# Optimization experiments

Measured on AMD Instinct MI355X. Metric: run time of the kernel, lower is better.

Reference implementation:

```python
import jax, jax.numpy as jnp
import numpy as np

T, B, I, H = 4096, 32, 128, 128


def setup_inputs() -> dict:
    key = jax.random.key(0)
    ks = jax.random.split(key, 8)
    return {
        "input": jax.random.normal(ks[0], (T, B, I), dtype=jnp.float32),
        "h0": jax.random.normal(ks[1], (B, H), dtype=jnp.float32),
        "c0": jax.random.normal(ks[2], (B, H), dtype=jnp.float32),
        "noise": jax.random.normal(ks[3], (B, H), dtype=jnp.float32),
        "W_ih": jax.random.normal(ks[4], (4 * H, I), dtype=jnp.float32) * 0.05,
        "W_hh": jax.random.normal(ks[5], (4 * H, H), dtype=jnp.float32) * 0.05,
        "b_ih": jax.random.normal(ks[6], (4 * H,), dtype=jnp.float32) * 0.05,
        "b_hh": jax.random.normal(ks[7], (4 * H,), dtype=jnp.float32) * 0.05,
    }


def reference(input, h0, c0, noise, W_ih, W_hh, b_ih, b_hh):
    # NOTE: the source LSTMLayer never rebinds `state` inside its loop, so every
    # timestep applies the cell to the SAME initial (h0, c0). This is therefore a
    # time-batched (non-recurrent) LSTM-cell application -> fully vectorized over T.
    hsz = h0.shape[-1]
    # gates: [T, B, 4H]
    gates = (
        jnp.einsum("tbi,gi->tbg", input, W_ih)
        + jnp.einsum("bh,gh->bg", h0, W_hh)[None, :, :]
        + (b_ih + b_hh)
    )
    i_g = jax.nn.sigmoid(gates[..., 0 * hsz : 1 * hsz])
    f_g = jax.nn.sigmoid(gates[..., 1 * hsz : 2 * hsz])
    g_g = jnp.tanh(gates[..., 2 * hsz : 3 * hsz])
    o_g = jax.nn.sigmoid(gates[..., 3 * hsz : 4 * hsz])
    c = f_g * c0[None] + i_g * g_g               # [T, B, H]
    h = o_g * jnp.tanh(c) + noise[None]          # [T, B, H] (additive process noise)
    outputs = h
    # (h, c) returned by the torch loop are those of the LAST iteration
    return (outputs, (h[-1], c[-1]))
```

## Files before the change

kernel.cpp:

```cpp
#include <hip/hip_runtime.h>
#include <hip/hip_bf16.h>

#define T_DIM 4096
#define B_DIM 32
#define H_DIM 128
#define M_DIM (T_DIM * B_DIM)
#define G_DIM 512
#define TBH   ((long)M_DIM * H_DIM)

#define RPB    512
#define NCHUNK (RPB / 32)
#define LSTR   136
#define LBUF   (32 * LSTR)

typedef __attribute__((ext_vector_type(8))) short short8;
typedef __attribute__((ext_vector_type(4))) short short4v;
typedef __attribute__((ext_vector_type(4))) float floatx4;

__device__ __forceinline__ unsigned short f2bf_rne(float x) {
    union { float f; unsigned int u; } v; v.f = x;
    unsigned int r = v.u + 0x7FFFu + ((v.u >> 16) & 1u);
    return (unsigned short)(r >> 16);
}
__device__ __forceinline__ unsigned short f2bf_rh(float x) {
    union { float f; unsigned int u; } v; v.f = x;
    return (unsigned short)((v.u + 0x8000u) >> 16);
}
__device__ __forceinline__ float sigm(float x) {
    return __builtin_amdgcn_rcpf(1.0f + __expf(-x));
}
__device__ __forceinline__ float tanh_fast(float x) {
    float e = __expf(-2.0f * __builtin_fabsf(x));
    float t = (1.0f - e) * __builtin_amdgcn_rcpf(1.0f + e);
    return __builtin_copysignf(t, x);
}
__device__ __forceinline__ short8 pack8(float4 f0, float4 f1) {
    short8 s;
    s[0] = (short)f2bf_rh(f0.x); s[1] = (short)f2bf_rh(f0.y);
    s[2] = (short)f2bf_rh(f0.z); s[3] = (short)f2bf_rh(f0.w);
    s[4] = (short)f2bf_rh(f1.x); s[5] = (short)f2bf_rh(f1.y);
    s[6] = (short)f2bf_rh(f1.z); s[7] = (short)f2bf_rh(f1.w);
    return s;
}

__global__ void prep(const float* __restrict__ h0,
                     const float* __restrict__ W_hh,
                     const float* __restrict__ b_ih,
                     const float* __restrict__ b_hh,
                     const float* __restrict__ W_ih,
                     unsigned short* __restrict__ Wb,
                     float* __restrict__ hh) {
    const int tid = threadIdx.x;
    if (blockIdx.x < 32) {
        __shared__ float h0s[128];
        const int b = blockIdx.x;
        if (tid < 128) h0s[tid] = h0[b * 128 + tid];
        __syncthreads();
        for (int g = tid; g < G_DIM; g += 256) {
            float acc = b_ih[g] + b_hh[g];
            const float* wr = W_hh + g * 128;
            #pragma unroll 8
            for (int k = 0; k < 128; ++k) acc += wr[k] * h0s[k];
            hh[b * G_DIM + g] = acc;
        }
    } else {
        const int e = ((blockIdx.x - 32) * 256 + tid) * 4;
        float4 f = *(const float4*)(W_ih + e);
        short4v s;
        s[0] = (short)f2bf_rne(f.x); s[1] = (short)f2bf_rne(f.y);
        s[2] = (short)f2bf_rne(f.z); s[3] = (short)f2bf_rne(f.w);
        *(short4v*)(Wb + e) = s;
    }
}

__global__ __launch_bounds__(512, 2) void lstm_main(
    const float* __restrict__ X,
    const unsigned short* __restrict__ W,
    const float* __restrict__ hh,
    const float* __restrict__ c0,
    const float* __restrict__ noise,
    float* __restrict__ out)
{
    __shared__ unsigned short Xs[2 * LBUF];

    const int tid  = threadIdx.x;
    const int w    = tid >> 6;
    const int lane = tid & 63;
    const int q    = lane >> 4;
    const int lr   = lane & 15;
    const int hcol = (w << 4) + lr;
    const long row0 = (long)blockIdx.x * RPB;

    short8 wf[4][4];
    #pragma unroll
    for (int g = 0; g < 4; ++g)
        #pragma unroll
        for (int kt = 0; kt < 4; ++kt)
            wf[g][kt] = *(const short8*)(W + (g * 128 + hcol) * 128 + kt * 32 + q * 8);

    floatx4 hhf[2][4];
    float c0v[2][4], nzv[2][4];
    #pragma unroll
    for (int mt = 0; mt < 2; ++mt) {
        #pragma unroll
        for (int r = 0; r < 4; ++r) {
            const int b = mt * 16 + q * 4 + r;
            c0v[mt][r] = c0[b * 128 + hcol];
            nzv[mt][r] = noise[b * 128 + hcol];
        }
        #pragma unroll
        for (int g = 0; g < 4; ++g) {
            floatx4 a;
            #pragma unroll
            for (int r = 0; r < 4; ++r)
                a[r] = hh[(mt * 16 + q * 4 + r) * G_DIM + g * 128 + hcol];
            hhf[mt][g] = a;
        }
    }

    const int srow = tid >> 4;
    const int scol = (tid & 15) << 3;
    const float* xsrc = X + (row0 + srow) * 128 + scol;
    unsigned short* lws = &Xs[srow * LSTR + scol];

    {
        float4 f0 = *(const float4*)(xsrc);
        float4 f1 = *(const float4*)(xsrc + 4);
        *(short8*)lws = pack8(f0, f1);
    }
    float4 p0 = *(const float4*)(xsrc + 4096);
    float4 p1 = *(const float4*)(xsrc + 4096 + 4);
    __syncthreads();

    for (int c = 0; c < NCHUNK; ++c) {
        float4 n0 = {}, n1 = {};
        if (c + 2 < NCHUNK) {
            n0 = *(const float4*)(xsrc + (long)(c + 2) * 4096);
            n1 = *(const float4*)(xsrc + (long)(c + 2) * 4096 + 4);
        }

        const unsigned short* rb = &Xs[(c & 1) * LBUF];
        short8 af[2][4];
        #pragma unroll
        for (int mt = 0; mt < 2; ++mt)
            #pragma unroll
            for (int kt = 0; kt < 4; ++kt)
                af[mt][kt] = *(const short8*)(rb + (mt * 16 + lr) * LSTR + kt * 32 + q * 8);

        floatx4 acc[2][4];
        #pragma unroll
        for (int mt = 0; mt < 2; ++mt)
            #pragma unroll
            for (int g = 0; g < 4; ++g)
                acc[mt][g] = hhf[mt][g];

        #pragma unroll
        for (int kt = 0; kt < 4; ++kt)
            #pragma unroll
            for (int g = 0; g < 4; ++g) {
                acc[0][g] = __builtin_amdgcn_mfma_f32_16x16x32_bf16(af[0][kt], wf[g][kt], acc[0][g], 0, 0, 0);
                acc[1][g] = __builtin_amdgcn_mfma_f32_16x16x32_bf16(af[1][kt], wf[g][kt], acc[1][g], 0, 0, 0);
            }

        const long rbase = row0 + (long)c * 32;
        const bool last = (rbase == M_DIM - 32);
        #pragma unroll
        for (int mt = 0; mt < 2; ++mt)
            #pragma unroll
            for (int r = 0; r < 4; ++r) {
                const long row = rbase + mt * 16 + q * 4 + r;
                const float gi = sigm(acc[mt][0][r]);
                const float gf = sigm(acc[mt][1][r]);
                const float gg = tanh_fast(acc[mt][2][r]);
                const float go = sigm(acc[mt][3][r]);
                const float cc = gf * c0v[mt][r] + gi * gg;
                const float hv = go * tanh_fast(cc) + nzv[mt][r];
                out[row * 128 + hcol] = hv;
                if (last) {
                    const int b = mt * 16 + q * 4 + r;
                    out[TBH +        b * 128 + hcol] = hv;
                    out[TBH + 4096 + b * 128 + hcol] = cc;
                }
            }

        if (c + 1 < NCHUNK)
            *(short8*)(lws + ((c + 1) & 1) * LBUF) = pack8(p0, p1);
        __syncthreads();
        p0 = n0; p1 = n1;
    }
}

extern "C" void kernel_launch(void* const* d_in, const int* in_sizes, int n_in,
                              void* d_out, int out_size, void* d_ws, size_t ws_size,
                              hipStream_t stream) {
    const float* X     = (const float*)d_in[0];
    const float* h0    = (const float*)d_in[1];
    const float* c0    = (const float*)d_in[2];
    const float* noise = (const float*)d_in[3];
    const float* W_ih  = (const float*)d_in[4];
    const float* W_hh  = (const float*)d_in[5];
    const float* b_ih  = (const float*)d_in[6];
    const float* b_hh  = (const float*)d_in[7];

    unsigned short* Wb = (unsigned short*)d_ws;
    float* hh = (float*)((char*)d_ws + 512 * 128 * sizeof(unsigned short));
    float* out = (float*)d_out;

    prep<<<dim3(96), dim3(256), 0, stream>>>(h0, W_hh, b_ih, b_hh, W_ih, Wb, hh);
    lstm_main<<<dim3(M_DIM / RPB), dim3(512), 0, stream>>>(X, Wb, hh, c0, noise, out);
}
```

Before: 150.6 us.

## Software-pipeline MFMA of next chunk with epilogue of previous chunk

Restructures the main loop into a two-accumulator ping-pong so the MFMA for chunk c+1 is issued before the transcendental epilogue and stores of chunk c. The aim is to overlap matrix-core work with VALU activation math and global stores, which the old loop ran back-to-back. It doubles the live accumulator registers, which may raise VGPR pressure under launch_bounds(512,2) and risk spills or lower occupancy.

```diff
diff --git a/kernel.cpp b/kernel.cpp
--- a/kernel.cpp
+++ b/kernel.cpp
@@ -16,6 +16,8 @@
 typedef __attribute__((ext_vector_type(8))) short short8;
 typedef __attribute__((ext_vector_type(4))) short short4v;
 typedef __attribute__((ext_vector_type(4))) float floatx4;
+
+struct F8 { float4 a, b; };
 
 __device__ __forceinline__ unsigned short f2bf_rne(float x) {
     union { float f; unsigned int u; } v; v.f = x;
@@ -123,37 +125,28 @@
     const float* xsrc = X + (row0 + srow) * 128 + scol;
     unsigned short* lws = &Xs[srow * LSTR + scol];
 
-    {
-        float4 f0 = *(const float4*)(xsrc);
-        float4 f1 = *(const float4*)(xsrc + 4);
-        *(short8*)lws = pack8(f0, f1);
-    }
-    float4 p0 = *(const float4*)(xsrc + 4096);
-    float4 p1 = *(const float4*)(xsrc + 4096 + 4);
-    __syncthreads();
-
-    for (int c = 0; c < NCHUNK; ++c) {
-        float4 n0 = {}, n1 = {};
-        if (c + 2 < NCHUNK) {
-            n0 = *(const float4*)(xsrc + (long)(c + 2) * 4096);
-            n1 = *(const float4*)(xsrc + (long)(c + 2) * 4096 + 4);
-        }
-
-        const unsigned short* rb = &Xs[(c & 1) * LBUF];
+    auto loadX = [&](int c) -> F8 {
+        F8 v;
+        v.a = *(const float4*)(xsrc + (long)c * 4096);
+        v.b = *(const float4*)(xsrc + (long)c * 4096 + 4);
+        return v;
+    };
+    auto stage_write = [&](int par, F8 v) {
+        *(short8*)(lws + par * LBUF) = pack8(v.a, v.b);
+    };
+    auto mfma_chunk = [&](floatx4 (&acc)[2][4], int par) {
+        const unsigned short* rb = &Xs[par * LBUF];
         short8 af[2][4];
         #pragma unroll
         for (int mt = 0; mt < 2; ++mt)
             #pragma unroll
             for (int kt = 0; kt < 4; ++kt)
                 af[mt][kt] = *(const short8*)(rb + (mt * 16 + lr) * LSTR + kt * 32 + q * 8);
-
-        floatx4 acc[2][4];
         #pragma unroll
         for (int mt = 0; mt < 2; ++mt)
             #pragma unroll
             for (int g = 0; g < 4; ++g)
                 acc[mt][g] = hhf[mt][g];
-
         #pragma unroll
         for (int kt = 0; kt < 4; ++kt)
             #pragma unroll
@@ -161,8 +154,8 @@
                 acc[0][g] = __builtin_amdgcn_mfma_f32_16x16x32_bf16(af[0][kt], wf[g][kt], acc[0][g], 0, 0, 0);
                 acc[1][g] = __builtin_amdgcn_mfma_f32_16x16x32_bf16(af[1][kt], wf[g][kt], acc[1][g], 0, 0, 0);
             }
-
-        const long rbase = row0 + (long)c * 32;
+    };
+    auto epilogue = [&](const floatx4 (&acc)[2][4], long rbase) {
         const bool last = (rbase == M_DIM - 32);
         #pragma unroll
         for (int mt = 0; mt < 2; ++mt)
@@ -182,12 +175,43 @@
                     out[TBH + 4096 + b * 128 + hcol] = cc;
                 }
             }
-
-        if (c + 1 < NCHUNK)
-            *(short8*)(lws + ((c + 1) & 1) * LBUF) = pack8(p0, p1);
+    };
+
+    floatx4 accA[2][4], accB[2][4];
+
+    {
+        F8 v0;
+        v0.a = *(const float4*)(xsrc);
+        v0.b = *(const float4*)(xsrc + 4);
+        stage_write(0, v0);
+    }
+    F8 p = loadX(1);
+    __syncthreads();
+    mfma_chunk(accA, 0);
+    stage_write(1, p);
+    p = loadX(2);
+    __syncthreads();
+
+    #pragma unroll 1
+    for (int c = 1; c + 2 < NCHUNK; c += 2) {
+        F8 n = loadX(c + 2);
+        mfma_chunk(accB, 1);
+        epilogue(accA, row0 + (long)(c - 1) * 32);
+        stage_write(0, p);
         __syncthreads();
-        p0 = n0; p1 = n1;
-    }
+        p = n;
+        F8 n2 = {};
+        if (c + 3 < NCHUNK) n2 = loadX(c + 3);
+        mfma_chunk(accA, 0);
+        epilogue(accB, row0 + (long)c * 32);
+        stage_write(1, p);
+        __syncthreads();
+        p = n2;
+    }
+
+    mfma_chunk(accB, 1);
+    epilogue(accA, row0 + (long)(NCHUNK - 2) * 32);
+    epilogue(accB, row0 + (long)(NCHUNK - 1) * 32);
 }
 
 extern "C" void kernel_launch(void* const* d_in, const int* in_sizes, int n_in,
```

New measurement: 150.5 us. No clear change (-0.1%).

## Split hidden columns across two blocks with 256 threads each

Applied to the files above, without the earlier changes.

Each block now handles 64 of the 128 hidden columns using 4 waves instead of 8, and the grid doubles to cover both column halves. Each thread stages 16 input elements per chunk instead of 8. The intent is more blocks in flight for better occupancy and latency hiding. The cost is that each input row chunk is read and converted to bf16 by two blocks, doubling X traffic into the caches.

```diff
diff --git a/kernel.cpp b/kernel.cpp
--- a/kernel.cpp
+++ b/kernel.cpp
@@ -73,7 +73,7 @@
     }
 }
 
-__global__ __launch_bounds__(512, 2) void lstm_main(
+__global__ __launch_bounds__(256, 2) void lstm_main(
     const float* __restrict__ X,
     const unsigned short* __restrict__ W,
     const float* __restrict__ hh,
@@ -88,8 +88,9 @@
     const int lane = tid & 63;
     const int q    = lane >> 4;
     const int lr   = lane & 15;
-    const int hcol = (w << 4) + lr;
-    const long row0 = (long)blockIdx.x * RPB;
+    const int colhalf = blockIdx.x & 1;
+    const int hcol = colhalf * 64 + (w << 4) + lr;
+    const long row0 = (long)(blockIdx.x >> 1) * RPB;
 
     short8 wf[4][4];
     #pragma unroll
@@ -118,25 +119,33 @@
         }
     }
 
-    const int srow = tid >> 4;
-    const int scol = (tid & 15) << 3;
+    const int srow = tid >> 3;
+    const int scol = (tid & 7) << 4;
     const float* xsrc = X + (row0 + srow) * 128 + scol;
     unsigned short* lws = &Xs[srow * LSTR + scol];
 
     {
         float4 f0 = *(const float4*)(xsrc);
         float4 f1 = *(const float4*)(xsrc + 4);
-        *(short8*)lws = pack8(f0, f1);
+        float4 f2 = *(const float4*)(xsrc + 8);
+        float4 f3 = *(const float4*)(xsrc + 12);
+        *(short8*)lws       = pack8(f0, f1);
+        *(short8*)(lws + 8) = pack8(f2, f3);
     }
     float4 p0 = *(const float4*)(xsrc + 4096);
     float4 p1 = *(const float4*)(xsrc + 4096 + 4);
+    float4 p2 = *(const float4*)(xsrc + 4096 + 8);
+    float4 p3 = *(const float4*)(xsrc + 4096 + 12);
     __syncthreads();
 
     for (int c = 0; c < NCHUNK; ++c) {
-        float4 n0 = {}, n1 = {};
+        float4 n0 = {}, n1 = {}, n2 = {}, n3 = {};
         if (c + 2 < NCHUNK) {
-            n0 = *(const float4*)(xsrc + (long)(c + 2) * 4096);
-            n1 = *(const float4*)(xsrc + (long)(c + 2) * 4096 + 4);
+            const float* s2 = xsrc + (long)(c + 2) * 4096;
+            n0 = *(const float4*)(s2);
+            n1 = *(const float4*)(s2 + 4);
+            n2 = *(const float4*)(s2 + 8);
+            n3 = *(const float4*)(s2 + 12);
         }
 
         const unsigned short* rb = &Xs[(c & 1) * LBUF];
@@ -183,10 +192,13 @@
                 }
             }
 
-        if (c + 1 < NCHUNK)
-            *(short8*)(lws + ((c + 1) & 1) * LBUF) = pack8(p0, p1);
+        if (c + 1 < NCHUNK) {
+            unsigned short* d = lws + ((c + 1) & 1) * LBUF;
+            *(short8*)d       = pack8(p0, p1);
+            *(short8*)(d + 8) = pack8(p2, p3);
+        }
         __syncthreads();
-        p0 = n0; p1 = n1;
+        p0 = n0; p1 = n1; p2 = n2; p3 = n3;
     }
 }
 
@@ -207,5 +219,5 @@
     float* out = (float*)d_out;
 
     prep<<<dim3(96), dim3(256), 0, stream>>>(h0, W_hh, b_ih, b_hh, W_ih, Wb, hh);
-    lstm_main<<<dim3(M_DIM / RPB), dim3(512), 0, stream>>>(X, Wb, hh, c0, noise, out);
-}
+    lstm_main<<<dim3((M_DIM / RPB) * 2), dim3(256), 0, stream>>>(X, Wb, hh, c0, noise, out);
+}
```

New measurement: 158.9 us. 1.06x slower.
